# Kernel optimization log

Measured on AMD Instinct MI355X. Metric: run time of the kernel, lower is better.

## Reference

```python
import jax, jax.numpy as jnp
import numpy as np

N_NODES = 100000
N_EDGES = 1600000
DIM_IN, DIM_H, DIM_OUT = 64, 64, 16


def setup_inputs() -> dict:
    key = jax.random.key(0)
    ks = jax.random.split(key, 7)
    s = lambda d: 1.0 / np.sqrt(d)
    return {
        "x": jax.random.normal(ks[0], (N_NODES, DIM_IN), dtype=jnp.float32),
        "edge_index": jax.random.randint(ks[1], (2, N_EDGES), 0, N_NODES, dtype=jnp.int32),
        "W1l": jax.random.normal(ks[2], (DIM_IN, DIM_H), dtype=jnp.float32) * s(DIM_IN),
        "W1r": jax.random.normal(ks[3], (DIM_IN, DIM_H), dtype=jnp.float32) * s(DIM_IN),
        "b1": jnp.zeros((DIM_H,), dtype=jnp.float32),
        "W2l": jax.random.normal(ks[4], (DIM_H, DIM_OUT), dtype=jnp.float32) * s(DIM_H),
        "W2r": jax.random.normal(ks[5], (DIM_H, DIM_OUT), dtype=jnp.float32) * s(DIM_H),
        "b2": jnp.zeros((DIM_OUT,), dtype=jnp.float32),
    }


def _sage_conv(h, edge_index, Wl, Wr, b):
    # PyG SAGEConv (mean aggr): out = mean_{j in N(i)} h_j @ Wl + h_i @ Wr + b
    src, dst = edge_index[0], edge_index[1]
    n = h.shape[0]
    agg = jax.ops.segment_sum(h[src], dst, num_segments=n)          # [N, d]
    deg = jax.ops.segment_sum(jnp.ones_like(dst, dtype=h.dtype), dst, num_segments=n)
    mean = agg / jnp.maximum(deg, 1.0)[:, None]
    return mean @ Wl + h @ Wr + b


def reference(x, edge_index, W1l, W1r, b1, W2l, W2r, b2):
    h = jax.nn.relu(_sage_conv(x, edge_index, W1l, W1r, b1))
    # dropout(p=0.5) is identity in eval mode (training=False)
    h = _sage_conv(h, edge_index, W2l, W2r, b2)
    return jax.nn.log_softmax(h, axis=1)
```

## Files before the change

### kernel.cpp

```cpp
#include <hip/hip_runtime.h>
#include <cstdint>
#include <cstddef>


typedef float f32x4 __attribute__((ext_vector_type(4)));
typedef float f32x2 __attribute__((ext_vector_type(2)));
typedef short short8 __attribute__((ext_vector_type(8)));
typedef __bf16 bf16x8 __attribute__((ext_vector_type(8)));

#define BK 256
#define NBMAX 512
#define CAP 5120
#define TILE 8192

__device__ __forceinline__ unsigned f2bf(float f) {
    unsigned u = __float_as_uint(f);
    u += 0x7FFFu + ((u >> 16) & 1u);
    return u >> 16;
}

__device__ __forceinline__ f32x4 mfma16(short8 a, short8 b, f32x4 c) {
    return __builtin_amdgcn_mfma_f32_16x16x32_bf16(
        __builtin_bit_cast(bf16x8, a), __builtin_bit_cast(bf16x8, b), c, 0, 0, 0);
}

#define ACC2(r, alo, ahi)                     \
    alo += __uint_as_float((r) << 16);        \
    ahi += __uint_as_float(r);

#define ACCF8(w, i)                                                   \
    {                                                                 \
        f32x2 f0 = __builtin_amdgcn_cvt_pk_f32_fp8((w), false);       \
        f32x2 f1 = __builtin_amdgcn_cvt_pk_f32_fp8((w), true);        \
        acc[(i)] += f0.x; acc[(i) + 1] += f0.y;                       \
        acc[(i) + 2] += f1.x; acc[(i) + 3] += f1.y;                   \
    }

__global__ __launch_bounds__(512) void partprep_k(
    const int* __restrict__ ei, int* __restrict__ bcnt,
    unsigned* __restrict__ part, int E, int pblocks,
    const float* __restrict__ x, unsigned short* __restrict__ xb,
    unsigned char* __restrict__ xqA, unsigned char* __restrict__ xqB, int n,
    const float* __restrict__ W1l, const float* __restrict__ W1r,
    const float* __restrict__ W2l, const float* __restrict__ W2r,
    unsigned short* __restrict__ bimg, int xblocks) {
    __shared__ int scn[NBMAX], sbase[NBMAX], lofs[NBMAX], cur[NBMAX];
    __shared__ unsigned stageW[TILE];
    __shared__ unsigned short stageB[TILE];
    int t = threadIdx.x;
    int bid = blockIdx.x;

    if (bid >= pblocks) {
        int cb = bid - pblocks;
        if (cb < xblocks) {
            int i = (cb * 512 + t) * 8;
            if (i >= n) return;
            const float4* xp = (const float4*)(x + i);
            float4 a = xp[0], b = xp[1];
            uint4 o;
            o.x = f2bf(a.x) | (f2bf(a.y) << 16);
            o.y = f2bf(a.z) | (f2bf(a.w) << 16);
            o.z = f2bf(b.x) | (f2bf(b.y) << 16);
            o.w = f2bf(b.z) | (f2bf(b.w) << 16);
            *(uint4*)(xb + i) = o;
            int w0 = __builtin_amdgcn_cvt_pk_fp8_f32(a.x, a.y, 0, false);
            w0 = __builtin_amdgcn_cvt_pk_fp8_f32(a.z, a.w, w0, true);
            int w1 = __builtin_amdgcn_cvt_pk_fp8_f32(b.x, b.y, 0, false);
            w1 = __builtin_amdgcn_cvt_pk_fp8_f32(b.z, b.w, w1, true);
            int node = i >> 6, feat = i & 63;
            unsigned char* dst = (feat < 32) ? (xqA + (size_t)node * 32 + feat)
                                             : (xqB + (size_t)node * 32 + (feat - 32));
            *(uint2*)dst = make_uint2((unsigned)w0, (unsigned)w1);
            return;
        }
        int e = (cb - xblocks) * 512 + t;
        if (e >= 20 * 64) return;
        int f = e >> 6, L = e & 63;
        int qd = L >> 4, m = L & 15;
        unsigned o[8];
        if (f < 16) {
            int kb = f >> 2, nb = f & 3;
            int n2 = nb * 16 + m;
#pragma unroll
            for (int j = 0; j < 8; ++j) {
                int k = kb * 32 + qd * 8 + j;
                float v = (k < 64) ? W1l[k * 64 + n2] : W1r[(k - 64) * 64 + n2];
                o[j] = f2bf(v);
            }
        } else {
            int g = f - 16;
            int kb = g >> 1, nb = g & 1;
#pragma unroll
            for (int j = 0; j < 8; ++j) {
                int k = kb * 32 + qd * 8 + j;
                float v = nb ? W2r[k * 16 + m] : W2l[k * 16 + m];
                o[j] = f2bf(v);
            }
        }
        uint4 pk;
        pk.x = o[0] | (o[1] << 16);
        pk.y = o[2] | (o[3] << 16);
        pk.z = o[4] | (o[5] << 16);
        pk.w = o[6] | (o[7] << 16);
        ((uint4*)bimg)[e] = pk;
        return;
    }

    int base = bid * TILE;
    cur[t] = 0;
    __syncthreads();
    int4 s4[4], d4[4];
#pragma unroll
    for (int i = 0; i < 4; ++i) {
        int e0 = base + (t + i * 512) * 4;
        if (e0 < E) {
            s4[i] = ((const int4*)ei)[e0 >> 2];
            d4[i] = ((const int4*)(ei + E))[e0 >> 2];
        } else {
            d4[i] = make_int4(-1, -1, -1, -1);
            s4[i] = make_int4(0, 0, 0, 0);
        }
    }
    int rk[16];
#pragma unroll
    for (int i = 0; i < 4; ++i) {
        int d[4] = {d4[i].x, d4[i].y, d4[i].z, d4[i].w};
#pragma unroll
        for (int u = 0; u < 4; ++u)
            rk[i * 4 + u] = (d[u] >= 0) ? atomicAdd(&cur[d[u] >> 8], 1) : 0;
    }
    __syncthreads();
    int own = cur[t];
    scn[t] = own;
    __syncthreads();
    for (int off = 1; off < NBMAX; off <<= 1) {
        int v = (t >= off) ? scn[t - off] : 0;
        __syncthreads();
        scn[t] += v;
        __syncthreads();
    }
    lofs[t] = scn[t] - own;
    if (own > 0) sbase[t] = atomicAdd(&bcnt[t], own);
    __syncthreads();
#pragma unroll
    for (int i = 0; i < 4; ++i) {
        int s[4] = {s4[i].x, s4[i].y, s4[i].z, s4[i].w};
        int d[4] = {d4[i].x, d4[i].y, d4[i].z, d4[i].w};
#pragma unroll
        for (int u = 0; u < 4; ++u) {
            if (d[u] < 0) continue;
            int b = d[u] >> 8;
            int pos = lofs[b] + rk[i * 4 + u];
            stageW[pos] = ((unsigned)(d[u] & (BK - 1)) << 17) | (unsigned)s[u];
            stageB[pos] = (unsigned short)b;
        }
    }
    __syncthreads();
    int tot = scn[NBMAX - 1];
    for (int q = t; q < tot; q += 512) {
        int b = stageB[q];
        part[b * CAP + sbase[b] + (q - lofs[b])] = stageW[q];
    }
}

__global__ __launch_bounds__(256) void csr_k(const unsigned* __restrict__ part,
                                             const int* __restrict__ bcnt,
                                             int* __restrict__ csr,
                                             int2* __restrict__ rowse, int N) {
    __shared__ int h[BK];
    __shared__ int s[BK];
    int b = blockIdx.x, t = threadIdx.x;
    int cnt = bcnt[b];
    int base = b * CAP;
    h[t] = 0;
    __syncthreads();
    for (int q = t; q < cnt; q += 256)
        atomicAdd(&h[(part[base + q] >> 17) & (BK - 1)], 1);
    __syncthreads();
    int own = h[t];
    s[t] = own;
    __syncthreads();
    for (int off = 1; off < BK; off <<= 1) {
        int v = (t >= off) ? s[t - off] : 0;
        __syncthreads();
        s[t] += v;
        __syncthreads();
    }
    int excl = s[t] - own;
    int node = b * BK + t;
    if (node < N) rowse[node] = make_int2(base + excl, base + excl + own);
    __syncthreads();
    h[t] = excl;
    __syncthreads();
    for (int q = t; q < cnt; q += 256) {
        unsigned w = part[base + q];
        int pos = atomicAdd(&h[(w >> 17) & (BK - 1)], 1);
        csr[base + pos] = (int)(w & 0x1FFFFu);
    }
}

__global__ __launch_bounds__(256) void gathA(
    const unsigned char* __restrict__ xqA, const int2* __restrict__ rowse,
    const int* __restrict__ csr, unsigned short* __restrict__ meanA, int N) {
    int t = threadIdx.x;
    int wave = t >> 6, lane = t & 63;
    int grp = lane >> 2, sub = lane & 3;
    int node = blockIdx.x * 64 + wave * 16 + grp;
    if (node >= N) return;
    int2 be = rowse[node];
    float acc[8];
#pragma unroll
    for (int i = 0; i < 8; ++i) acc[i] = 0.f;
    int k = be.x, kend = be.y;
    for (; k + 3 < kend; k += 4) {
        int s0 = csr[k], s1 = csr[k + 1], s2 = csr[k + 2], s3 = csr[k + 3];
        uint2 a = *(const uint2*)(xqA + ((size_t)s0 << 5) + (sub << 3));
        uint2 b = *(const uint2*)(xqA + ((size_t)s1 << 5) + (sub << 3));
        uint2 c = *(const uint2*)(xqA + ((size_t)s2 << 5) + (sub << 3));
        uint2 d = *(const uint2*)(xqA + ((size_t)s3 << 5) + (sub << 3));
        ACCF8(a.x, 0); ACCF8(a.y, 4);
        ACCF8(b.x, 0); ACCF8(b.y, 4);
        ACCF8(c.x, 0); ACCF8(c.y, 4);
        ACCF8(d.x, 0); ACCF8(d.y, 4);
    }
    if (k + 1 < kend) {
        int s0 = csr[k], s1 = csr[k + 1];
        uint2 a = *(const uint2*)(xqA + ((size_t)s0 << 5) + (sub << 3));
        uint2 b = *(const uint2*)(xqA + ((size_t)s1 << 5) + (sub << 3));
        ACCF8(a.x, 0); ACCF8(a.y, 4);
        ACCF8(b.x, 0); ACCF8(b.y, 4);
        k += 2;
    }
    if (k < kend) {
        int s0 = csr[k];
        uint2 a = *(const uint2*)(xqA + ((size_t)s0 << 5) + (sub << 3));
        ACCF8(a.x, 0); ACCF8(a.y, 4);
    }
    float rd = 1.0f / fmaxf((float)(be.y - be.x), 1.0f);
    uint4 o;
    o.x = f2bf(acc[0] * rd) | (f2bf(acc[1] * rd) << 16);
    o.y = f2bf(acc[2] * rd) | (f2bf(acc[3] * rd) << 16);
    o.z = f2bf(acc[4] * rd) | (f2bf(acc[5] * rd) << 16);
    o.w = f2bf(acc[6] * rd) | (f2bf(acc[7] * rd) << 16);
    *(uint4*)(meanA + ((size_t)node << 5) + (sub << 3)) = o;
}

__global__ __launch_bounds__(256, 4) void l1x(
    const unsigned short* __restrict__ xb, const unsigned char* __restrict__ xqB,
    const unsigned short* __restrict__ meanA,
    const int2* __restrict__ rowse, const int* __restrict__ csr,
    const unsigned short* __restrict__ bimg,
    const float* __restrict__ b1, const float* __restrict__ b2,
    unsigned short* __restrict__ p, float* __restrict__ q, int N) {
    __shared__ unsigned short mh[4][16][72];
    int t = threadIdx.x;
    int wave = t >> 6, lane = t & 63;
    int nodebase = blockIdx.x * 64 + wave * 16;
    int grp = lane >> 2, sub = lane & 3;
    int node = nodebase + grp;
    int2 be = (node < N) ? rowse[node] : make_int2(0, 0);

    float acc[8];
#pragma unroll
    for (int i = 0; i < 8; ++i) acc[i] = 0.f;
    int k = be.x, kend = be.y;
    for (; k + 3 < kend; k += 4) {
        int s0 = csr[k], s1 = csr[k + 1], s2 = csr[k + 2], s3 = csr[k + 3];
        uint2 a = *(const uint2*)(xqB + ((size_t)s0 << 5) + (sub << 3));
        uint2 b = *(const uint2*)(xqB + ((size_t)s1 << 5) + (sub << 3));
        uint2 c = *(const uint2*)(xqB + ((size_t)s2 << 5) + (sub << 3));
        uint2 d = *(const uint2*)(xqB + ((size_t)s3 << 5) + (sub << 3));
        ACCF8(a.x, 0); ACCF8(a.y, 4);
        ACCF8(b.x, 0); ACCF8(b.y, 4);
        ACCF8(c.x, 0); ACCF8(c.y, 4);
        ACCF8(d.x, 0); ACCF8(d.y, 4);
    }
    if (k + 1 < kend) {
        int s0 = csr[k], s1 = csr[k + 1];
        uint2 a = *(const uint2*)(xqB + ((size_t)s0 << 5) + (sub << 3));
        uint2 b = *(const uint2*)(xqB + ((size_t)s1 << 5) + (sub << 3));
        ACCF8(a.x, 0); ACCF8(a.y, 4);
        ACCF8(b.x, 0); ACCF8(b.y, 4);
        k += 2;
    }
    if (k < kend) {
        int s0 = csr[k];
        uint2 a = *(const uint2*)(xqB + ((size_t)s0 << 5) + (sub << 3));
        ACCF8(a.x, 0); ACCF8(a.y, 4);
    }
    {
        float rd = 1.0f / fmaxf((float)(be.y - be.x), 1.0f);
        uint4 o;
        o.x = f2bf(acc[0] * rd) | (f2bf(acc[1] * rd) << 16);
        o.y = f2bf(acc[2] * rd) | (f2bf(acc[3] * rd) << 16);
        o.z = f2bf(acc[4] * rd) | (f2bf(acc[5] * rd) << 16);
        o.w = f2bf(acc[6] * rd) | (f2bf(acc[7] * rd) << 16);
        *(uint4*)&mh[wave][grp][sub * 8] = o;
    }

    int qd = lane >> 4, m = lane & 15;
    int mynode = nodebase + m;
    const short8* bfr = (const short8*)bimg;
    short8 afr0 = {0, 0, 0, 0, 0, 0, 0, 0};
    short8 afr1 = *(const short8*)&mh[wave][m][qd * 8];
    short8 afr2 = {0, 0, 0, 0, 0, 0, 0, 0};
    short8 afr3 = {0, 0, 0, 0, 0, 0, 0, 0};
    if (mynode < N) {
        afr0 = *(const short8*)(meanA + ((size_t)mynode << 5) + qd * 8);
        afr2 = *(const short8*)(xb + ((size_t)mynode << 6) + qd * 8);
        afr3 = *(const short8*)(xb + ((size_t)mynode << 6) + 32 + qd * 8);
    }

#pragma unroll
    for (int nb = 0; nb < 4; ++nb) {
        f32x4 c = {0.f, 0.f, 0.f, 0.f};
        c = mfma16(afr0, bfr[nb * 64 + lane], c);
        c = mfma16(afr1, bfr[(4 + nb) * 64 + lane], c);
        c = mfma16(afr2, bfr[(8 + nb) * 64 + lane], c);
        c = mfma16(afr3, bfr[(12 + nb) * 64 + lane], c);
        int col = nb * 16 + m;
        float bb = b1[col];
#pragma unroll
        for (int r = 0; r < 4; ++r) {
            float hv = fmaxf(c[r] + bb, 0.0f);
            mh[wave][qd * 4 + r][col] = (unsigned short)f2bf(hv);
        }
    }

    short8 ha0 = *(const short8*)&mh[wave][m][qd * 8];
    short8 ha1 = *(const short8*)&mh[wave][m][32 + qd * 8];
    f32x4 pc = {0.f, 0.f, 0.f, 0.f}, qc = {0.f, 0.f, 0.f, 0.f};
    pc = mfma16(ha0, bfr[16 * 64 + lane], pc);
    pc = mfma16(ha1, bfr[18 * 64 + lane], pc);
    qc = mfma16(ha0, bfr[17 * 64 + lane], qc);
    qc = mfma16(ha1, bfr[19 * 64 + lane], qc);
    float b2v = b2[m];
#pragma unroll
    for (int r = 0; r < 4; ++r) {
        int nd = nodebase + qd * 4 + r;
        if (nd < N) {
            p[(size_t)nd * 16 + m] = (unsigned short)f2bf(pc[r]);
            q[(size_t)nd * 16 + m] = qc[r] + b2v;
        }
    }
}

__global__ __launch_bounds__(256) void finalk(const unsigned short* __restrict__ p,
                                              const int2* __restrict__ rowse,
                                              const int* __restrict__ csr,
                                              float* q, int N) {
    int t = threadIdx.x;
    int wave = t >> 6, lane = t & 63;
    int grp = lane >> 2, sub = lane & 3;
    int node = blockIdx.x * 64 + wave * 16 + grp;
    if (node >= N) return;
    int2 be = rowse[node];
    float4 qv = ((const float4*)(q + ((size_t)node << 4)))[sub];
    float a0 = 0.f, a1 = 0.f, a2 = 0.f, a3 = 0.f;
    int k = be.x, kend = be.y;
    for (; k + 3 < kend; k += 4) {
        int s0 = csr[k], s1 = csr[k + 1], s2 = csr[k + 2], s3 = csr[k + 3];
        uint2 rA = *(const uint2*)(p + ((size_t)s0 << 4) + (sub << 2));
        uint2 rB = *(const uint2*)(p + ((size_t)s1 << 4) + (sub << 2));
        uint2 rC = *(const uint2*)(p + ((size_t)s2 << 4) + (sub << 2));
        uint2 rD = *(const uint2*)(p + ((size_t)s3 << 4) + (sub << 2));
        ACC2(rA.x, a0, a1);  ACC2(rA.y, a2, a3);
        ACC2(rB.x, a0, a1);  ACC2(rB.y, a2, a3);
        ACC2(rC.x, a0, a1);  ACC2(rC.y, a2, a3);
        ACC2(rD.x, a0, a1);  ACC2(rD.y, a2, a3);
    }
    if (k + 1 < kend) {
        int s0 = csr[k], s1 = csr[k + 1];
        uint2 rA = *(const uint2*)(p + ((size_t)s0 << 4) + (sub << 2));
        uint2 rB = *(const uint2*)(p + ((size_t)s1 << 4) + (sub << 2));
        ACC2(rA.x, a0, a1);  ACC2(rA.y, a2, a3);
        ACC2(rB.x, a0, a1);  ACC2(rB.y, a2, a3);
        k += 2;
    }
    if (k < kend) {
        int s0 = csr[k];
        uint2 rA = *(const uint2*)(p + ((size_t)s0 << 4) + (sub << 2));
        ACC2(rA.x, a0, a1);  ACC2(rA.y, a2, a3);
    }
    float rd = 1.0f / fmaxf((float)(be.y - be.x), 1.0f);
    float4 v = {a0 * rd + qv.x, a1 * rd + qv.y, a2 * rd + qv.z, a3 * rd + qv.w};
    float mm = fmaxf(fmaxf(v.x, v.y), fmaxf(v.z, v.w));
    mm = fmaxf(mm, __shfl_xor(mm, 1));
    mm = fmaxf(mm, __shfl_xor(mm, 2));
    float s = __expf(v.x - mm) + __expf(v.y - mm) + __expf(v.z - mm) + __expf(v.w - mm);
    s += __shfl_xor(s, 1);
    s += __shfl_xor(s, 2);
    float ls = __logf(s);
    float4 o = {v.x - mm - ls, v.y - mm - ls, v.z - mm - ls, v.w - mm - ls};
    ((float4*)(q + ((size_t)node << 4)))[sub] = o;
}

extern "C" void kernel_launch(void* const* d_in, const int* in_sizes, int n_in,
                              void* d_out, int out_size, void* d_ws, size_t ws_size,
                              hipStream_t stream) {
    const float* x   = (const float*)d_in[0];
    const int* ei    = (const int*)d_in[1];
    const float* W1l = (const float*)d_in[2];
    const float* W1r = (const float*)d_in[3];
    const float* b1  = (const float*)d_in[4];
    const float* W2l = (const float*)d_in[5];
    const float* W2r = (const float*)d_in[6];
    const float* b2  = (const float*)d_in[7];
    const int N = in_sizes[0] / 64;
    const int E = in_sizes[1] / 2;
    const int nbk = (N + BK - 1) / BK;

    int*  bcnt  = (int*)d_ws;
    int2* rowse = (int2*)(bcnt + NBMAX);
    int*  csr   = (int*)(rowse + N);
    unsigned short* bimg = (unsigned short*)(csr + (size_t)nbk * CAP);
    unsigned short* p    = bimg + 20 * 64 * 8;
    unsigned* part = (unsigned*)(p + (size_t)N * 16);
    unsigned short* meanA = (unsigned short*)part;
    unsigned short* xb = (unsigned short*)(part + (size_t)nbk * CAP);
    unsigned char* xqA = (unsigned char*)(xb + (size_t)N * 64);
    unsigned char* xqB = xqA + (size_t)N * 32;
    float* q = (float*)d_out;

    hipMemsetAsync(bcnt, 0, NBMAX * sizeof(int), stream);

    const int pblocks = (E + TILE - 1) / TILE;
    const int xblocks = (N * 64 + 4095) / 4096;
    partprep_k<<<pblocks + xblocks + 3, 512, 0, stream>>>(
        ei, bcnt, part, E, pblocks, x, xb, xqA, xqB, N * 64, W1l, W1r, W2l,
        W2r, bimg, xblocks);
    csr_k<<<nbk, 256, 0, stream>>>(part, bcnt, csr, rowse, N);
    gathA<<<(N + 63) / 64, 256, 0, stream>>>(xqA, rowse, csr, meanA, N);
    l1x<<<(N + 63) / 64, 256, 0, stream>>>(xb, xqB, meanA, rowse, csr, bimg,
                                           b1, b2, p, q, N);
    finalk<<<(N + 63) / 64, 256, 0, stream>>>(p, rowse, csr, q, N);
}
```

Measured before the change: 170.5 us.

## Fuse first-half neighbor gather into l1x and use nontemporal loads/stores

Removes the separate gathA kernel and its meanA intermediate. l1x now gathers both 32-column halves (xqA and xqB) in two passes over the same CSR row and places both halves in shared memory for the MFMA layer. CSR, rowse, xb and the outputs are read and written with nontemporal hints, and launch bounds move from 4 to 6 blocks per CU. This saves one launch plus the meanA write and read, but walks the CSR indices twice in one kernel and raises register pressure.

```diff
diff --git a/kernel.cpp b/kernel.cpp
--- a/kernel.cpp
+++ b/kernel.cpp
@@ -7,6 +7,8 @@
 typedef float f32x2 __attribute__((ext_vector_type(2)));
 typedef short short8 __attribute__((ext_vector_type(8)));
 typedef __bf16 bf16x8 __attribute__((ext_vector_type(8)));
+typedef unsigned uv2 __attribute__((ext_vector_type(2)));
+typedef int iv2 __attribute__((ext_vector_type(2)));
 
 #define BK 256
 #define NBMAX 512
@@ -199,55 +201,9 @@
     }
 }
 
-__global__ __launch_bounds__(256) void gathA(
-    const unsigned char* __restrict__ xqA, const int2* __restrict__ rowse,
-    const int* __restrict__ csr, unsigned short* __restrict__ meanA, int N) {
-    int t = threadIdx.x;
-    int wave = t >> 6, lane = t & 63;
-    int grp = lane >> 2, sub = lane & 3;
-    int node = blockIdx.x * 64 + wave * 16 + grp;
-    if (node >= N) return;
-    int2 be = rowse[node];
-    float acc[8];
-#pragma unroll
-    for (int i = 0; i < 8; ++i) acc[i] = 0.f;
-    int k = be.x, kend = be.y;
-    for (; k + 3 < kend; k += 4) {
-        int s0 = csr[k], s1 = csr[k + 1], s2 = csr[k + 2], s3 = csr[k + 3];
-        uint2 a = *(const uint2*)(xqA + ((size_t)s0 << 5) + (sub << 3));
-        uint2 b = *(const uint2*)(xqA + ((size_t)s1 << 5) + (sub << 3));
-        uint2 c = *(const uint2*)(xqA + ((size_t)s2 << 5) + (sub << 3));
-        uint2 d = *(const uint2*)(xqA + ((size_t)s3 << 5) + (sub << 3));
-        ACCF8(a.x, 0); ACCF8(a.y, 4);
-        ACCF8(b.x, 0); ACCF8(b.y, 4);
-        ACCF8(c.x, 0); ACCF8(c.y, 4);
-        ACCF8(d.x, 0); ACCF8(d.y, 4);
-    }
-    if (k + 1 < kend) {
-        int s0 = csr[k], s1 = csr[k + 1];
-        uint2 a = *(const uint2*)(xqA + ((size_t)s0 << 5) + (sub << 3));
-        uint2 b = *(const uint2*)(xqA + ((size_t)s1 << 5) + (sub << 3));
-        ACCF8(a.x, 0); ACCF8(a.y, 4);
-        ACCF8(b.x, 0); ACCF8(b.y, 4);
-        k += 2;
-    }
-    if (k < kend) {
-        int s0 = csr[k];
-        uint2 a = *(const uint2*)(xqA + ((size_t)s0 << 5) + (sub << 3));
-        ACCF8(a.x, 0); ACCF8(a.y, 4);
-    }
-    float rd = 1.0f / fmaxf((float)(be.y - be.x), 1.0f);
-    uint4 o;
-    o.x = f2bf(acc[0] * rd) | (f2bf(acc[1] * rd) << 16);
-    o.y = f2bf(acc[2] * rd) | (f2bf(acc[3] * rd) << 16);
-    o.z = f2bf(acc[4] * rd) | (f2bf(acc[5] * rd) << 16);
-    o.w = f2bf(acc[6] * rd) | (f2bf(acc[7] * rd) << 16);
-    *(uint4*)(meanA + ((size_t)node << 5) + (sub << 3)) = o;
-}
-
-__global__ __launch_bounds__(256, 4) void l1x(
-    const unsigned short* __restrict__ xb, const unsigned char* __restrict__ xqB,
-    const unsigned short* __restrict__ meanA,
+__global__ __launch_bounds__(256, 6) void l1x(
+    const unsigned short* __restrict__ xb,
+    const unsigned char* __restrict__ xqA, const unsigned char* __restrict__ xqB,
     const int2* __restrict__ rowse, const int* __restrict__ csr,
     const unsigned short* __restrict__ bimg,
     const float* __restrict__ b1, const float* __restrict__ b2,
@@ -258,38 +214,43 @@
     int nodebase = blockIdx.x * 64 + wave * 16;
     int grp = lane >> 2, sub = lane & 3;
     int node = nodebase + grp;
-    int2 be = (node < N) ? rowse[node] : make_int2(0, 0);
+    iv2 be = {0, 0};
+    if (node < N) be = __builtin_nontemporal_load((const iv2*)(rowse + node));
+    float rd = 1.0f / fmaxf((float)(be[1] - be[0]), 1.0f);
 
     float acc[8];
 #pragma unroll
     for (int i = 0; i < 8; ++i) acc[i] = 0.f;
-    int k = be.x, kend = be.y;
-    for (; k + 3 < kend; k += 4) {
-        int s0 = csr[k], s1 = csr[k + 1], s2 = csr[k + 2], s3 = csr[k + 3];
-        uint2 a = *(const uint2*)(xqB + ((size_t)s0 << 5) + (sub << 3));
-        uint2 b = *(const uint2*)(xqB + ((size_t)s1 << 5) + (sub << 3));
-        uint2 c = *(const uint2*)(xqB + ((size_t)s2 << 5) + (sub << 3));
-        uint2 d = *(const uint2*)(xqB + ((size_t)s3 << 5) + (sub << 3));
-        ACCF8(a.x, 0); ACCF8(a.y, 4);
-        ACCF8(b.x, 0); ACCF8(b.y, 4);
-        ACCF8(c.x, 0); ACCF8(c.y, 4);
-        ACCF8(d.x, 0); ACCF8(d.y, 4);
-    }
-    if (k + 1 < kend) {
-        int s0 = csr[k], s1 = csr[k + 1];
-        uint2 a = *(const uint2*)(xqB + ((size_t)s0 << 5) + (sub << 3));
-        uint2 b = *(const uint2*)(xqB + ((size_t)s1 << 5) + (sub << 3));
-        ACCF8(a.x, 0); ACCF8(a.y, 4);
-        ACCF8(b.x, 0); ACCF8(b.y, 4);
-        k += 2;
-    }
-    if (k < kend) {
-        int s0 = csr[k];
-        uint2 a = *(const uint2*)(xqB + ((size_t)s0 << 5) + (sub << 3));
-        ACCF8(a.x, 0); ACCF8(a.y, 4);
-    }
     {
-        float rd = 1.0f / fmaxf((float)(be.y - be.x), 1.0f);
+        int k = be[0], kend = be[1];
+        for (; k + 3 < kend; k += 4) {
+            int s0 = __builtin_nontemporal_load(csr + k);
+            int s1 = __builtin_nontemporal_load(csr + k + 1);
+            int s2 = __builtin_nontemporal_load(csr + k + 2);
+            int s3 = __builtin_nontemporal_load(csr + k + 3);
+            uv2 a = *(const uv2*)(xqA + ((size_t)s0 << 5) + (sub << 3));
+            uv2 b = *(const uv2*)(xqA + ((size_t)s1 << 5) + (sub << 3));
+            uv2 c = *(const uv2*)(xqA + ((size_t)s2 << 5) + (sub << 3));
+            uv2 d = *(const uv2*)(xqA + ((size_t)s3 << 5) + (sub << 3));
+            ACCF8(a[0], 0); ACCF8(a[1], 4);
+            ACCF8(b[0], 0); ACCF8(b[1], 4);
+            ACCF8(c[0], 0); ACCF8(c[1], 4);
+            ACCF8(d[0], 0); ACCF8(d[1], 4);
+        }
+        if (k + 1 < kend) {
+            int s0 = __builtin_nontemporal_load(csr + k);
+            int s1 = __builtin_nontemporal_load(csr + k + 1);
+            uv2 a = *(const uv2*)(xqA + ((size_t)s0 << 5) + (sub << 3));
+            uv2 b = *(const uv2*)(xqA + ((size_t)s1 << 5) + (sub << 3));
+            ACCF8(a[0], 0); ACCF8(a[1], 4);
+            ACCF8(b[0], 0); ACCF8(b[1], 4);
+            k += 2;
+        }
+        if (k < kend) {
+            int s0 = __builtin_nontemporal_load(csr + k);
+            uv2 a = *(const uv2*)(xqA + ((size_t)s0 << 5) + (sub << 3));
+            ACCF8(a[0], 0); ACCF8(a[1], 4);
+        }
         uint4 o;
         o.x = f2bf(acc[0] * rd) | (f2bf(acc[1] * rd) << 16);
         o.y = f2bf(acc[2] * rd) | (f2bf(acc[3] * rd) << 16);
@@ -297,18 +258,58 @@
         o.w = f2bf(acc[6] * rd) | (f2bf(acc[7] * rd) << 16);
         *(uint4*)&mh[wave][grp][sub * 8] = o;
     }
+#pragma unroll
+    for (int i = 0; i < 8; ++i) acc[i] = 0.f;
+    {
+        int k = be[0], kend = be[1];
+        for (; k + 3 < kend; k += 4) {
+            int s0 = __builtin_nontemporal_load(csr + k);
+            int s1 = __builtin_nontemporal_load(csr + k + 1);
+            int s2 = __builtin_nontemporal_load(csr + k + 2);
+            int s3 = __builtin_nontemporal_load(csr + k + 3);
+            uv2 a = *(const uv2*)(xqB + ((size_t)s0 << 5) + (sub << 3));
+            uv2 b = *(const uv2*)(xqB + ((size_t)s1 << 5) + (sub << 3));
+            uv2 c = *(const uv2*)(xqB + ((size_t)s2 << 5) + (sub << 3));
+            uv2 d = *(const uv2*)(xqB + ((size_t)s3 << 5) + (sub << 3));
+            ACCF8(a[0], 0); ACCF8(a[1], 4);
+            ACCF8(b[0], 0); ACCF8(b[1], 4);
+            ACCF8(c[0], 0); ACCF8(c[1], 4);
+            ACCF8(d[0], 0); ACCF8(d[1], 4);
+        }
+        if (k + 1 < kend) {
+            int s0 = __builtin_nontemporal_load(csr + k);
+            int s1 = __builtin_nontemporal_load(csr + k + 1);
+            uv2 a = *(const uv2*)(xqB + ((size_t)s0 << 5) + (sub << 3));
+            uv2 b = *(const uv2*)(xqB + ((size_t)s1 << 5) + (sub << 3));
+            ACCF8(a[0], 0); ACCF8(a[1], 4);
+            ACCF8(b[0], 0); ACCF8(b[1], 4);
+            k += 2;
+        }
+        if (k < kend) {
+            int s0 = __builtin_nontemporal_load(csr + k);
+            uv2 a = *(const uv2*)(xqB + ((size_t)s0 << 5) + (sub << 3));
+            ACCF8(a[0], 0); ACCF8(a[1], 4);
+        }
+        uint4 o;
+        o.x = f2bf(acc[0] * rd) | (f2bf(acc[1] * rd) << 16);
+        o.y = f2bf(acc[2] * rd) | (f2bf(acc[3] * rd) << 16);
+        o.z = f2bf(acc[4] * rd) | (f2bf(acc[5] * rd) << 16);
+        o.w = f2bf(acc[6] * rd) | (f2bf(acc[7] * rd) << 16);
+        *(uint4*)&mh[wave][grp][32 + sub * 8] = o;
+    }
 
     int qd = lane >> 4, m = lane & 15;
     int mynode = nodebase + m;
     const short8* bfr = (const short8*)bimg;
-    short8 afr0 = {0, 0, 0, 0, 0, 0, 0, 0};
-    short8 afr1 = *(const short8*)&mh[wave][m][qd * 8];
+    short8 afr0 = *(const short8*)&mh[wave][m][qd * 8];
+    short8 afr1 = *(const short8*)&mh[wave][m][32 + qd * 8];
     short8 afr2 = {0, 0, 0, 0, 0, 0, 0, 0};
     short8 afr3 = {0, 0, 0, 0, 0, 0, 0, 0};
     if (mynode < N) {
-        afr0 = *(const short8*)(meanA + ((size_t)mynode << 5) + qd * 8);
-        afr2 = *(const short8*)(xb + ((size_t)mynode << 6) + qd * 8);
-        afr3 = *(const short8*)(xb + ((size_t)mynode << 6) + 32 + qd * 8);
+        afr2 = __builtin_nontemporal_load(
+            (const short8*)(xb + ((size_t)mynode << 6) + qd * 8));
+        afr3 = __builtin_nontemporal_load(
+            (const short8*)(xb + ((size_t)mynode << 6) + 32 + qd * 8));
     }
 
 #pragma unroll
@@ -339,8 +340,9 @@
     for (int r = 0; r < 4; ++r) {
         int nd = nodebase + qd * 4 + r;
         if (nd < N) {
-            p[(size_t)nd * 16 + m] = (unsigned short)f2bf(pc[r]);
-            q[(size_t)nd * 16 + m] = qc[r] + b2v;
+            __builtin_nontemporal_store((unsigned short)f2bf(pc[r]),
+                                        p + ((size_t)nd << 4) + m);
+            __builtin_nontemporal_store(qc[r] + b2v, q + ((size_t)nd << 4) + m);
         }
     }
 }
@@ -354,12 +356,16 @@
     int grp = lane >> 2, sub = lane & 3;
     int node = blockIdx.x * 64 + wave * 16 + grp;
     if (node >= N) return;
-    int2 be = rowse[node];
-    float4 qv = ((const float4*)(q + ((size_t)node << 4)))[sub];
+    iv2 be = __builtin_nontemporal_load((const iv2*)(rowse + node));
+    f32x4 qv = __builtin_nontemporal_load(
+        (const f32x4*)(q + ((size_t)node << 4) + (sub << 2)));
     float a0 = 0.f, a1 = 0.f, a2 = 0.f, a3 = 0.f;
-    int k = be.x, kend = be.y;
+    int k = be[0], kend = be[1];
     for (; k + 3 < kend; k += 4) {
-        int s0 = csr[k], s1 = csr[k + 1], s2 = csr[k + 2], s3 = csr[k + 3];
+        int s0 = __builtin_nontemporal_load(csr + k);
+        int s1 = __builtin_nontemporal_load(csr + k + 1);
+        int s2 = __builtin_nontemporal_load(csr + k + 2);
+        int s3 = __builtin_nontemporal_load(csr + k + 3);
         uint2 rA = *(const uint2*)(p + ((size_t)s0 << 4) + (sub << 2));
         uint2 rB = *(const uint2*)(p + ((size_t)s1 << 4) + (sub << 2));
         uint2 rC = *(const uint2*)(p + ((size_t)s2 << 4) + (sub << 2));
@@ -370,7 +376,8 @@
         ACC2(rD.x, a0, a1);  ACC2(rD.y, a2, a3);
     }
     if (k + 1 < kend) {
-        int s0 = csr[k], s1 = csr[k + 1];
+        int s0 = __builtin_nontemporal_load(csr + k);
+        int s1 = __builtin_nontemporal_load(csr + k + 1);
         uint2 rA = *(const uint2*)(p + ((size_t)s0 << 4) + (sub << 2));
         uint2 rB = *(const uint2*)(p + ((size_t)s1 << 4) + (sub << 2));
         ACC2(rA.x, a0, a1);  ACC2(rA.y, a2, a3);
@@ -378,21 +385,21 @@
         k += 2;
     }
     if (k < kend) {
-        int s0 = csr[k];
+        int s0 = __builtin_nontemporal_load(csr + k);
         uint2 rA = *(const uint2*)(p + ((size_t)s0 << 4) + (sub << 2));
         ACC2(rA.x, a0, a1);  ACC2(rA.y, a2, a3);
     }
-    float rd = 1.0f / fmaxf((float)(be.y - be.x), 1.0f);
-    float4 v = {a0 * rd + qv.x, a1 * rd + qv.y, a2 * rd + qv.z, a3 * rd + qv.w};
-    float mm = fmaxf(fmaxf(v.x, v.y), fmaxf(v.z, v.w));
+    float rd = 1.0f / fmaxf((float)(be[1] - be[0]), 1.0f);
+    f32x4 v = {a0 * rd + qv[0], a1 * rd + qv[1], a2 * rd + qv[2], a3 * rd + qv[3]};
+    float mm = fmaxf(fmaxf(v[0], v[1]), fmaxf(v[2], v[3]));
     mm = fmaxf(mm, __shfl_xor(mm, 1));
     mm = fmaxf(mm, __shfl_xor(mm, 2));
-    float s = __expf(v.x - mm) + __expf(v.y - mm) + __expf(v.z - mm) + __expf(v.w - mm);
+    float s = __expf(v[0] - mm) + __expf(v[1] - mm) + __expf(v[2] - mm) + __expf(v[3] - mm);
     s += __shfl_xor(s, 1);
     s += __shfl_xor(s, 2);
     float ls = __logf(s);
-    float4 o = {v.x - mm - ls, v.y - mm - ls, v.z - mm - ls, v.w - mm - ls};
-    ((float4*)(q + ((size_t)node << 4)))[sub] = o;
+    f32x4 o = {v[0] - mm - ls, v[1] - mm - ls, v[2] - mm - ls, v[3] - mm - ls};
+    __builtin_nontemporal_store(o, (f32x4*)(q + ((size_t)node << 4) + (sub << 2)));
 }
 
 extern "C" void kernel_launch(void* const* d_in, const int* in_sizes, int n_in,
@@ -416,7 +423,6 @@
     unsigned short* bimg = (unsigned short*)(csr + (size_t)nbk * CAP);
     unsigned short* p    = bimg + 20 * 64 * 8;
     unsigned* part = (unsigned*)(p + (size_t)N * 16);
-    unsigned short* meanA = (unsigned short*)part;
     unsigned short* xb = (unsigned short*)(part + (size_t)nbk * CAP);
     unsigned char* xqA = (unsigned char*)(xb + (size_t)N * 64);
     unsigned char* xqB = xqA + (size_t)N * 32;
@@ -430,8 +436,7 @@
         ei, bcnt, part, E, pblocks, x, xb, xqA, xqB, N * 64, W1l, W1r, W2l,
         W2r, bimg, xblocks);
     csr_k<<<nbk, 256, 0, stream>>>(part, bcnt, csr, rowse, N);
-    gathA<<<(N + 63) / 64, 256, 0, stream>>>(xqA, rowse, csr, meanA, N);
-    l1x<<<(N + 63) / 64, 256, 0, stream>>>(xb, xqB, meanA, rowse, csr, bimg,
+    l1x<<<(N + 63) / 64, 256, 0, stream>>>(xb, xqA, xqB, rowse, csr, bimg,
                                            b1, b2, p, q, N);
     finalk<<<(N + 63) / 64, 256, 0, stream>>>(p, rowse, csr, q, N);
 }
```

Result: slower. 182.7 us (+7.2%).
